# Optimization experiments

Measured on AMD Instinct MI355X. Metric: run time of the kernel, lower is better.

## Reference

```python
import jax, jax.numpy as jnp
import numpy as np

B, S, D, H, E, K = 4, 2048, 768, 3072, 8, 2
CAP_FACTOR = 1.5


def setup_inputs() -> dict:
    key = jax.random.key(0)
    ks = jax.random.split(key, 6)
    x = jax.random.normal(ks[0], (B, S, D), jnp.float32)
    Wr = jax.random.normal(ks[1], (D, E), jnp.float32) * 0.01  # router, std=0.01 init
    w1 = jax.random.normal(ks[2], (E, D, H), jnp.float32) * (1.0 / np.sqrt(D))
    b1 = jnp.zeros((E, H), jnp.float32)
    w2 = jax.random.normal(ks[3], (E, H, D), jnp.float32) * (1.0 / np.sqrt(H))
    b2 = jnp.zeros((E, D), jnp.float32)
    return {"x": x, "Wr": Wr, "w1": w1, "b1": b1, "w2": w2, "b2": b2}


def _moe_forward(x, Wr, w1, b1, w2, b2):
    Bz, Sz, Dz = x.shape
    Ez = Wr.shape[1]
    capacity = int((Bz * Sz / Ez) * CAP_FACTOR)  # 1536

    # --- Router (eval mode: no jitter, no dropout) ---
    logits = x @ Wr                                # [B,S,E]
    probs = jax.nn.softmax(logits, axis=-1)
    topk_p, topk_i = jax.lax.top_k(probs, K)       # [B,S,K]
    topk_p = topk_p / topk_p.sum(-1, keepdims=True)

    # --- Capacity-limited assignment, vectorized equivalent of the serial
    #     (b, s, i) loop: an entry is kept iff fewer than `capacity` earlier
    #     entries (in flat (b,s,i) order) chose the same expert. ---
    e_flat = topk_i.reshape(-1)                    # [N], N = B*S*K, i innermost
    p_flat = topk_p.reshape(-1)
    onehot = (e_flat[:, None] == jnp.arange(Ez)[None, :]).astype(x.dtype)  # [N,E]
    counts_before = jnp.cumsum(onehot, axis=0) - onehot                     # [N,E]
    pos = jnp.take_along_axis(counts_before, e_flat[:, None], axis=1)[:, 0]
    keep = (pos < capacity).astype(x.dtype)        # [N]

    # combine weight per (token, expert): sum over the k slots
    cw = (onehot * (p_flat * keep)[:, None]).reshape(Bz, Sz, K, Ez).sum(2)  # [B,S,E]

    # --- Expert FFNs (dense: every expert on every token, weighted combine) ---
    hidden = jax.nn.gelu(jnp.einsum('bsd,edh->bseh', x, w1) + b1, approximate=False)
    expert_out = jnp.einsum('bseh,ehd->bsed', hidden, w2) + b2               # [B,S,E,D]
    return jnp.einsum('bse,bsed->bsd', cw, expert_out)


def reference(x, Wr, w1, b1, w2, b2):
    return _moe_forward(x, Wr, w1, b1, w2, b2)
```

## Files before the change

### kernel.cpp

```cpp
#include <hip/hip_runtime.h>
#include <hip/hip_bf16.h>
#include <math.h>

#define TOK    8192
#define DMODEL 768
#define HDIM   3072
#define NEXP   8
#define CAP    1536
#define NFLAT  (TOK*2)

typedef __attribute__((ext_vector_type(8))) short bf16x8;
typedef __attribute__((ext_vector_type(4))) float f32x4;

static __device__ __forceinline__ unsigned short f2bf(float f) {
  unsigned int u = __float_as_uint(f);
  u += 0x7FFF + ((u >> 16) & 1);
  return (unsigned short)(u >> 16);
}

static __device__ __forceinline__ float fast_gelu(float v) {
  const float v2 = v * v;
  const float y2 = v * (1.59576912f + 0.07135534f * v2);
  const float e  = __expf(y2);
  return v - v * __builtin_amdgcn_rcpf(e + 1.0f);
}

__global__ __launch_bounds__(256)
void moe_router(const float* __restrict__ x, const float* __restrict__ Wr,
                int* __restrict__ eidx, float* __restrict__ pw)
{
  const int wid = threadIdx.x >> 6, lane = threadIdx.x & 63;
  const int t = blockIdx.x * 4 + wid;
  const float* xr = x + (size_t)t * DMODEL;
  double acc[NEXP];
#pragma unroll
  for (int e = 0; e < NEXP; ++e) acc[e] = 0.0;
  for (int j = 0; j < DMODEL / 64; ++j) {
    const int d = j * 64 + lane;
    const double xv = (double)xr[d];
    const float* wrow = Wr + (size_t)d * NEXP;
#pragma unroll
    for (int e = 0; e < NEXP; ++e) acc[e] += xv * (double)wrow[e];
  }
#pragma unroll
  for (int off = 32; off > 0; off >>= 1) {
#pragma unroll
    for (int e = 0; e < NEXP; ++e) acc[e] += __shfl_xor(acc[e], off, 64);
  }
  if (lane == 0) {
    int e0 = 0;
    for (int e = 1; e < NEXP; ++e) if (acc[e] > acc[e0]) e0 = e;
    int e1 = (e0 == 0) ? 1 : 0;
    for (int e = 0; e < NEXP; ++e) { if (e == e0) continue; if (acc[e] > acc[e1]) e1 = e; }
    const double p0 = 1.0 / (1.0 + exp(acc[e1] - acc[e0]));
    eidx[t * 2 + 0] = e0; eidx[t * 2 + 1] = e1;
    pw[t * 2 + 0] = (float)p0; pw[t * 2 + 1] = (float)(1.0 - p0);
  }
}

__global__ __launch_bounds__(256)
void moe_assign(const int* __restrict__ eidx, int* __restrict__ slotpos,
                int* __restrict__ elist, int* __restrict__ counts)
{
  const int e = blockIdx.x;
  const int tid = threadIdx.x;
  const int base = tid * 64;
  int cnt = 0;
  for (int j = 0; j < 64; ++j) cnt += (eidx[base + j] == e);
  const int lane = tid & 63, wid = tid >> 6;
  int incl = cnt;
  for (int off = 1; off < 64; off <<= 1) {
    int u = __shfl_up(incl, off, 64);
    if (lane >= off) incl += u;
  }
  __shared__ int wsum[4];
  if (lane == 63) wsum[wid] = incl;
  __syncthreads();
  int wbase = 0;
  for (int w = 0; w < wid; ++w) wbase += wsum[w];
  int run = wbase + incl - cnt;
  for (int j = 0; j < 64; ++j) {
    const int n = base + j;
    if (eidx[n] == e) {
      const int pos = run++;
      slotpos[n] = (pos < CAP) ? pos : -1;
      if (pos < CAP) elist[e * CAP + pos] = n >> 1;
    }
  }
  if (tid == 255) {
    int tot = wbase + incl;
    counts[e] = (tot < CAP) ? tot : CAP;
  }
}

__global__ __launch_bounds__(256)
void transpose_bf16(const float* __restrict__ in, unsigned short* __restrict__ out,
                    int R, int C)
{
  __shared__ unsigned short tile[64][65];
  const int e = blockIdx.z;
  in  += (size_t)e * R * C;
  out += (size_t)e * C * R;
  const int c0 = blockIdx.x * 64;
  const int r0 = blockIdx.y * 64;
  const int tid = threadIdx.x;
#pragma unroll
  for (int i = 0; i < 16; ++i) {
    const int L = tid + i * 256;
    const int r = L >> 6, c = L & 63;
    tile[r][c] = f2bf(in[(size_t)(r0 + r) * C + c0 + c]);
  }
  __syncthreads();
#pragma unroll
  for (int i = 0; i < 16; ++i) {
    const int L = tid + i * 256;
    const int rr = L & 63, cc = L >> 6;
    out[(size_t)(c0 + cc) * R + r0 + rr] = tile[rr][cc];
  }
}

__global__ __launch_bounds__(64)
void moe_gather(const float* __restrict__ x, const int* __restrict__ elist,
                const int* __restrict__ counts, unsigned short* __restrict__ Xg)
{
  const int p = blockIdx.x, e = blockIdx.y;
  const int lane = threadIdx.x;
  unsigned short* dst = Xg + ((size_t)e * CAP + p) * DMODEL;
  if (p >= counts[e]) {
    ushort4 z; z.x = z.y = z.z = z.w = 0;
#pragma unroll
    for (int j = 0; j < 3; ++j) ((ushort4*)dst)[j * 64 + lane] = z;
    return;
  }
  const int tok = elist[e * CAP + p];
  const float4* src = (const float4*)(x + (size_t)tok * DMODEL);
#pragma unroll
  for (int j = 0; j < 3; ++j) {
    float4 v = src[j * 64 + lane];
    ushort4 o;
    o.x = f2bf(v.x); o.y = f2bf(v.y); o.z = f2bf(v.z); o.w = f2bf(v.w);
    ((ushort4*)dst)[j * 64 + lane] = o;
  }
}

template <int EPI, int ORD>
__global__ __launch_bounds__(256)
void moe_rs(const unsigned short* __restrict__ Ag, int lda,
            const unsigned short* __restrict__ Bg, int ldb,
            void* __restrict__ Cout0, void* __restrict__ Cout1, int ldc,
            const float* __restrict__ bias,
            int Nsize, int NT, int MT, int NTN)
{
  __shared__ __align__(16) unsigned short lds[2 * 8192];
  unsigned short* const ldsA = lds;
  unsigned short* const ldsB = lds + 8192;

  const int cpx = gridDim.x >> 3;
  const int swz = (blockIdx.x & 7) * cpx + (blockIdx.x >> 3);
  const int e  = swz / cpx;
  int rd = swz - e * cpx;
  int mt, nt, ks;
  if (ORD == 0) { mt = rd % MT;  rd /= MT;  nt = rd % NTN; ks = rd / NTN; }
  else          { nt = rd % NTN; rd /= NTN; mt = rd % MT;  ks = rd / MT;  }
  const int m0 = mt * 128, n0 = nt * 128;
  const int kb = ks * NT * 64;

  const unsigned short* Ae = Ag + (size_t)e * CAP * lda;
  const unsigned short* Be = Bg + (size_t)e * Nsize * ldb;

  const int tid = threadIdx.x, lane = tid & 63, wid = tid >> 6;
  const int wr = wid >> 1, wc = wid & 1;
  const int r16 = lane & 15, g4 = lane >> 4;

  const int srow  = tid >> 3;
  const int scol  = tid & 7;
  const int scolX = scol ^ (srow & 7);
  const unsigned short* pA = Ae + (size_t)(m0 + srow) * lda + scol * 8 + kb;
  const unsigned short* pB = Be + (size_t)(n0 + srow) * ldb + scol * 8 + kb;
  unsigned short* qA = &ldsA[srow * 64 + scolX * 8];
  unsigned short* qB = &ldsB[srow * 64 + scolX * 8];

  float4 a0, a1, a2, a3, b0, b1, b2, b3;

#define LOADT(tt) do {                                                        \
    const size_t ko = (size_t)(tt) * 64;                                      \
    a0 = *(const float4*)(pA + ko);                                           \
    a1 = *(const float4*)(pA + ko + (size_t)32 * lda);                        \
    a2 = *(const float4*)(pA + ko + (size_t)64 * lda);                        \
    a3 = *(const float4*)(pA + ko + (size_t)96 * lda);                        \
    b0 = *(const float4*)(pB + ko);                                           \
    b1 = *(const float4*)(pB + ko + (size_t)32 * ldb);                        \
    b2 = *(const float4*)(pB + ko + (size_t)64 * ldb);                        \
    b3 = *(const float4*)(pB + ko + (size_t)96 * ldb);                        \
  } while (0)

#define STORET() do {                                                         \
    *(float4*)(qA)        = a0;  *(float4*)(qA + 2048) = a1;                  \
    *(float4*)(qA + 4096) = a2;  *(float4*)(qA + 6144) = a3;                  \
    *(float4*)(qB)        = b0;  *(float4*)(qB + 2048) = b1;                  \
    *(float4*)(qB + 4096) = b2;  *(float4*)(qB + 6144) = b3;                  \
  } while (0)

  f32x4 acc[4][4];
#pragma unroll
  for (int i = 0; i < 4; ++i)
#pragma unroll
    for (int j = 0; j < 4; ++j) acc[i][j] = (f32x4){0.f, 0.f, 0.f, 0.f};

  const int cx0 = (g4 ^ (r16 & 7)) * 8;
  const int rA = (wr * 64 + r16) * 64;
  const int rB = (wc * 64 + r16) * 64;

  LOADT(0);
  for (int t = 0; t < NT; ++t) {
    __syncthreads();
    STORET();
    if (t + 1 < NT) LOADT(t + 1);
    __syncthreads();
#pragma unroll
    for (int kh = 0; kh < 2; ++kh) {
      const int cx = cx0 ^ (kh * 32);
      bf16x8 aF[4], bF[4];
#pragma unroll
      for (int mi = 0; mi < 4; ++mi)
        aF[mi] = *(const bf16x8*)&ldsA[rA + mi * 1024 + cx];
#pragma unroll
      for (int ni = 0; ni < 4; ++ni)
        bF[ni] = *(const bf16x8*)&ldsB[rB + ni * 1024 + cx];
#pragma unroll
      for (int mi = 0; mi < 4; ++mi)
#pragma unroll
        for (int ni = 0; ni < 4; ++ni)
          acc[mi][ni] = __builtin_amdgcn_mfma_f32_16x16x32_bf16(aF[mi], bF[ni], acc[mi][ni], 0, 0, 0);
    }
  }
#undef LOADT
#undef STORET

  const float* bvec = bias + (size_t)e * Nsize;
  if constexpr (EPI == 0) {
    __syncthreads();
#pragma unroll
    for (int ni = 0; ni < 4; ++ni) {
      const int lc = wc * 64 + ni * 16 + r16;
      const float bv = bvec[n0 + lc];
#pragma unroll
      for (int mi = 0; mi < 4; ++mi) {
        const int lr0 = wr * 64 + mi * 16 + 4 * g4;
#pragma unroll
        for (int reg = 0; reg < 4; ++reg) {
          lds[(lr0 + reg) * 128 + lc] = f2bf(fast_gelu(acc[mi][ni][reg] + bv));
        }
      }
    }
    __syncthreads();
    unsigned short* C = (unsigned short*)Cout0 + (size_t)e * CAP * ldc;
#pragma unroll
    for (int it = 0; it < 8; ++it) {
      const int chunk = it * 256 + tid;
      const int row = chunk >> 4, c8 = chunk & 15;
      *(float4*)(C + (size_t)(m0 + row) * ldc + n0 + c8 * 8) = *(const float4*)&lds[chunk * 8];
    }
  } else {
    float* C = (float*)(ks ? Cout1 : Cout0) + (size_t)e * CAP * ldc;
#pragma unroll
    for (int ni = 0; ni < 4; ++ni) {
      const int gc = n0 + wc * 64 + ni * 16 + r16;
#pragma unroll
      for (int mi = 0; mi < 4; ++mi) {
        const int gr0 = m0 + wr * 64 + mi * 16 + 4 * g4;
#pragma unroll
        for (int reg = 0; reg < 4; ++reg)
          C[(size_t)(gr0 + reg) * ldc + gc] = acc[mi][ni][reg];
      }
    }
  }
}

__global__ __launch_bounds__(192)
void moe_combine(const float* __restrict__ Y0, const float* __restrict__ Y1,
                 const float* __restrict__ b2, const int* __restrict__ eidx,
                 const float* __restrict__ pw, const int* __restrict__ slotpos,
                 float* __restrict__ out)
{
  const int t = blockIdx.x;
  const int tid = threadIdx.x;
  float4 acc; acc.x = acc.y = acc.z = acc.w = 0.f;
#pragma unroll
  for (int s = 0; s < 2; ++s) {
    const int pos = slotpos[t * 2 + s];
    if (pos >= 0) {
      const int e = eidx[t * 2 + s];
      const float w = pw[t * 2 + s];
      const size_t ro = ((size_t)e * CAP + pos) * DMODEL;
      float4 y0 = ((const float4*)(Y0 + ro))[tid];
      float4 y1 = ((const float4*)(Y1 + ro))[tid];
      float4 bv = ((const float4*)(b2 + (size_t)e * DMODEL))[tid];
      acc.x += w * (y0.x + y1.x + bv.x);
      acc.y += w * (y0.y + y1.y + bv.y);
      acc.z += w * (y0.z + y1.z + bv.z);
      acc.w += w * (y0.w + y1.w + bv.w);
    }
  }
  ((float4*)out)[(size_t)t * (DMODEL / 4) + tid] = acc;
}

extern "C" void kernel_launch(void* const* d_in, const int* in_sizes, int n_in,
                              void* d_out, int out_size, void* d_ws, size_t ws_size,
                              hipStream_t stream)
{
  const float* x  = (const float*)d_in[0];
  const float* Wr = (const float*)d_in[1];
  const float* w1 = (const float*)d_in[2];
  const float* b1 = (const float*)d_in[3];
  const float* w2 = (const float*)d_in[4];
  const float* b2 = (const float*)d_in[5];
  float* out = (float*)d_out;

  char* ws = (char*)d_ws;
  const size_t SZ_W1T = (size_t)NEXP * HDIM * DMODEL * 2;
  const size_t SZ_W2T = (size_t)NEXP * DMODEL * HDIM * 2;
  const size_t SZ_XG  = (size_t)NEXP * CAP * DMODEL * 2;
  const size_t SZ_H   = (size_t)NEXP * CAP * HDIM * 2;
  const size_t SZ_Y   = (size_t)NEXP * CAP * DMODEL * 4;
  unsigned short* w1t = (unsigned short*)(ws);               size_t off = SZ_W1T;
  unsigned short* w2t = (unsigned short*)(ws + off);         off += SZ_W2T;
  unsigned short* Xg  = (unsigned short*)(ws + off);         off += SZ_XG;
  unsigned short* Hb  = (unsigned short*)(ws + off);         off += SZ_H;
  float*          Y0  = (float*)(ws + off);                  off += SZ_Y;
  int*   eidx    = (int*)(ws + off);                         off += (size_t)TOK * 2 * 4;
  float* pw      = (float*)(ws + off);                       off += (size_t)TOK * 2 * 4;
  int*   slotpos = (int*)(ws + off);                         off += (size_t)NFLAT * 4;
  int*   elist   = (int*)(ws + off);                         off += (size_t)NEXP * CAP * 4;
  int*   counts  = (int*)(ws + off);
  float* Y1 = (float*)w1t;

  moe_router<<<TOK / 4, 256, 0, stream>>>(x, Wr, eidx, pw);
  moe_assign<<<NEXP, 256, 0, stream>>>(eidx, slotpos, elist, counts);
  transpose_bf16<<<dim3(HDIM / 64, DMODEL / 64, NEXP), 256, 0, stream>>>(w1, w1t, DMODEL, HDIM);
  transpose_bf16<<<dim3(DMODEL / 64, HDIM / 64, NEXP), 256, 0, stream>>>(w2, w2t, HDIM, DMODEL);
  moe_gather<<<dim3(CAP, NEXP), 64, 0, stream>>>(x, elist, counts, Xg);
  moe_rs<0, 0><<<2304, 256, 0, stream>>>(
      Xg, DMODEL, w1t, DMODEL, Hb, Hb, HDIM, b1, HDIM, 12, 12, 24);
  moe_rs<1, 1><<<1152, 256, 0, stream>>>(
      Hb, HDIM, w2t, HDIM, Y0, Y1, DMODEL, b2, DMODEL, 24, 12, 6);
  moe_combine<<<TOK, 192, 0, stream>>>(Y0, Y1, b2, eidx, pw, slotpos, out);
}
```

Baseline: 244.7 us.

## Enlarge first expert GEMM tile to 256 rows and vectorize transpose/assign loads

The first expert GEMM now uses 256x128 tiles (MI=8 per wave), halving its grid and doubling reuse of each loaded weight tile. The GELU epilogue writes through LDS in two 128-row passes. The weight transpose kernel now uses float4 loads and ushort4 stores, and the assign kernel reads expert indices as int4. The larger tile raises accumulator register pressure (128 floats per thread) and LDS use, which may lower occupancy.

Result: slower. 730.6 us (+198.5%).

```diff
diff --git a/kernel.cpp b/kernel.cpp
--- a/kernel.cpp
+++ b/kernel.cpp
@@ -65,8 +65,13 @@
   const int e = blockIdx.x;
   const int tid = threadIdx.x;
   const int base = tid * 64;
+  const int4* p4 = (const int4*)(eidx + base);
   int cnt = 0;
-  for (int j = 0; j < 64; ++j) cnt += (eidx[base + j] == e);
+#pragma unroll
+  for (int j = 0; j < 16; ++j) {
+    int4 v = p4[j];
+    cnt += (v.x == e) + (v.y == e) + (v.z == e) + (v.w == e);
+  }
   const int lane = tid & 63, wid = tid >> 6;
   int incl = cnt;
   for (int off = 1; off < 64; off <<= 1) {
@@ -79,12 +84,18 @@
   int wbase = 0;
   for (int w = 0; w < wid; ++w) wbase += wsum[w];
   int run = wbase + incl - cnt;
-  for (int j = 0; j < 64; ++j) {
-    const int n = base + j;
-    if (eidx[n] == e) {
-      const int pos = run++;
-      slotpos[n] = (pos < CAP) ? pos : -1;
-      if (pos < CAP) elist[e * CAP + pos] = n >> 1;
+#pragma unroll
+  for (int j = 0; j < 16; ++j) {
+    int4 v = p4[j];
+    const int n = base + j * 4;
+    int vv[4] = {v.x, v.y, v.z, v.w};
+#pragma unroll
+    for (int q = 0; q < 4; ++q) {
+      if (vv[q] == e) {
+        const int pos = run++;
+        slotpos[n + q] = (pos < CAP) ? pos : -1;
+        if (pos < CAP) elist[e * CAP + pos] = (n + q) >> 1;
+      }
     }
   }
   if (tid == 255) {
@@ -101,21 +112,29 @@
   const int e = blockIdx.z;
   in  += (size_t)e * R * C;
   out += (size_t)e * C * R;
-  const int c0 = blockIdx.x * 64;
-  const int r0 = blockIdx.y * 64;
+  const int c0 = blockIdx.x * 64, r0 = blockIdx.y * 64;
   const int tid = threadIdx.x;
-#pragma unroll
-  for (int i = 0; i < 16; ++i) {
-    const int L = tid + i * 256;
-    const int r = L >> 6, c = L & 63;
-    tile[r][c] = f2bf(in[(size_t)(r0 + r) * C + c0 + c]);
+  const int rL = tid >> 4;
+  const int cq = (tid & 15) * 4;
+#pragma unroll
+  for (int p = 0; p < 4; ++p) {
+    const int r = rL + p * 16;
+    float4 v = *(const float4*)&in[(size_t)(r0 + r) * C + c0 + cq];
+    tile[r][cq + 0] = f2bf(v.x);
+    tile[r][cq + 1] = f2bf(v.y);
+    tile[r][cq + 2] = f2bf(v.z);
+    tile[r][cq + 3] = f2bf(v.w);
   }
   __syncthreads();
-#pragma unroll
-  for (int i = 0; i < 16; ++i) {
-    const int L = tid + i * 256;
-    const int rr = L & 63, cc = L >> 6;
-    out[(size_t)(c0 + cc) * R + r0 + rr] = tile[rr][cc];
+  const int cL = tid >> 4;
+  const int rq = (tid & 15) * 4;
+#pragma unroll
+  for (int p = 0; p < 4; ++p) {
+    const int cc = cL + p * 16;
+    ushort4 o;
+    o.x = tile[rq + 0][cc]; o.y = tile[rq + 1][cc];
+    o.z = tile[rq + 2][cc]; o.w = tile[rq + 3][cc];
+    *(ushort4*)&out[(size_t)(c0 + cc) * R + r0 + rq] = o;
   }
 }
 
@@ -143,7 +162,7 @@
   }
 }
 
-template <int EPI, int ORD>
+template <int EPI, int ORD, int MI>
 __global__ __launch_bounds__(256)
 void moe_rs(const unsigned short* __restrict__ Ag, int lda,
             const unsigned short* __restrict__ Bg, int ldb,
@@ -151,9 +170,11 @@
             const float* __restrict__ bias,
             int Nsize, int NT, int MT, int NTN)
 {
-  __shared__ __align__(16) unsigned short lds[2 * 8192];
+  constexpr int BM  = MI * 32;
+  constexpr int ASZ = BM * 64;
+  __shared__ __align__(16) unsigned short lds[ASZ + 8192];
   unsigned short* const ldsA = lds;
-  unsigned short* const ldsB = lds + 8192;
+  unsigned short* const ldsB = lds + ASZ;
 
   const int cpx = gridDim.x >> 3;
   const int swz = (blockIdx.x & 7) * cpx + (blockIdx.x >> 3);
@@ -162,7 +183,7 @@
   int mt, nt, ks;
   if (ORD == 0) { mt = rd % MT;  rd /= MT;  nt = rd % NTN; ks = rd / NTN; }
   else          { nt = rd % NTN; rd /= NTN; mt = rd % MT;  ks = rd / MT;  }
-  const int m0 = mt * 128, n0 = nt * 128;
+  const int m0 = mt * BM, n0 = nt * 128;
   const int kb = ks * NT * 64;
 
   const unsigned short* Ae = Ag + (size_t)e * CAP * lda;
@@ -180,35 +201,29 @@
   unsigned short* qA = &ldsA[srow * 64 + scolX * 8];
   unsigned short* qB = &ldsB[srow * 64 + scolX * 8];
 
-  float4 a0, a1, a2, a3, b0, b1, b2, b3;
-
-#define LOADT(tt) do {                                                        \
-    const size_t ko = (size_t)(tt) * 64;                                      \
-    a0 = *(const float4*)(pA + ko);                                           \
-    a1 = *(const float4*)(pA + ko + (size_t)32 * lda);                        \
-    a2 = *(const float4*)(pA + ko + (size_t)64 * lda);                        \
-    a3 = *(const float4*)(pA + ko + (size_t)96 * lda);                        \
-    b0 = *(const float4*)(pB + ko);                                           \
-    b1 = *(const float4*)(pB + ko + (size_t)32 * ldb);                        \
-    b2 = *(const float4*)(pB + ko + (size_t)64 * ldb);                        \
-    b3 = *(const float4*)(pB + ko + (size_t)96 * ldb);                        \
-  } while (0)
-
-#define STORET() do {                                                         \
-    *(float4*)(qA)        = a0;  *(float4*)(qA + 2048) = a1;                  \
-    *(float4*)(qA + 4096) = a2;  *(float4*)(qA + 6144) = a3;                  \
-    *(float4*)(qB)        = b0;  *(float4*)(qB + 2048) = b1;                  \
-    *(float4*)(qB + 4096) = b2;  *(float4*)(qB + 6144) = b3;                  \
-  } while (0)
-
-  f32x4 acc[4][4];
-#pragma unroll
-  for (int i = 0; i < 4; ++i)
+  float4 a[MI], b[4];
+  auto LOADT = [&](int tt) {
+    const size_t ko = (size_t)tt * 64;
+#pragma unroll
+    for (int j = 0; j < MI; ++j) a[j] = *(const float4*)(pA + ko + (size_t)(32 * j) * lda);
+#pragma unroll
+    for (int j = 0; j < 4; ++j)  b[j] = *(const float4*)(pB + ko + (size_t)(32 * j) * ldb);
+  };
+  auto STORET = [&]() {
+#pragma unroll
+    for (int j = 0; j < MI; ++j) *(float4*)(qA + j * 2048) = a[j];
+#pragma unroll
+    for (int j = 0; j < 4; ++j)  *(float4*)(qB + j * 2048) = b[j];
+  };
+
+  f32x4 acc[MI][4];
+#pragma unroll
+  for (int i = 0; i < MI; ++i)
 #pragma unroll
     for (int j = 0; j < 4; ++j) acc[i][j] = (f32x4){0.f, 0.f, 0.f, 0.f};
 
   const int cx0 = (g4 ^ (r16 & 7)) * 8;
-  const int rA = (wr * 64 + r16) * 64;
+  const int rA = (wr * (MI * 16) + r16) * 64;
   const int rB = (wc * 64 + r16) * 64;
 
   LOADT(0);
@@ -220,46 +235,50 @@
 #pragma unroll
     for (int kh = 0; kh < 2; ++kh) {
       const int cx = cx0 ^ (kh * 32);
-      bf16x8 aF[4], bF[4];
-#pragma unroll
-      for (int mi = 0; mi < 4; ++mi)
+      bf16x8 aF[MI], bF[4];
+#pragma unroll
+      for (int mi = 0; mi < MI; ++mi)
         aF[mi] = *(const bf16x8*)&ldsA[rA + mi * 1024 + cx];
 #pragma unroll
       for (int ni = 0; ni < 4; ++ni)
         bF[ni] = *(const bf16x8*)&ldsB[rB + ni * 1024 + cx];
 #pragma unroll
-      for (int mi = 0; mi < 4; ++mi)
+      for (int mi = 0; mi < MI; ++mi)
 #pragma unroll
         for (int ni = 0; ni < 4; ++ni)
           acc[mi][ni] = __builtin_amdgcn_mfma_f32_16x16x32_bf16(aF[mi], bF[ni], acc[mi][ni], 0, 0, 0);
     }
   }
-#undef LOADT
-#undef STORET
 
   const float* bvec = bias + (size_t)e * Nsize;
   if constexpr (EPI == 0) {
-    __syncthreads();
-#pragma unroll
-    for (int ni = 0; ni < 4; ++ni) {
-      const int lc = wc * 64 + ni * 16 + r16;
-      const float bv = bvec[n0 + lc];
-#pragma unroll
-      for (int mi = 0; mi < 4; ++mi) {
-        const int lr0 = wr * 64 + mi * 16 + 4 * g4;
-#pragma unroll
-        for (int reg = 0; reg < 4; ++reg) {
-          lds[(lr0 + reg) * 128 + lc] = f2bf(fast_gelu(acc[mi][ni][reg] + bv));
+    constexpr int NP = BM / 128;
+#pragma unroll
+    for (int p = 0; p < NP; ++p) {
+      __syncthreads();
+      if (NP == 1 || wr == p) {
+#pragma unroll
+        for (int ni = 0; ni < 4; ++ni) {
+          const int lc = wc * 64 + ni * 16 + r16;
+          const float bv = bvec[n0 + lc];
+#pragma unroll
+          for (int mi = 0; mi < MI; ++mi) {
+            const int lr0 = (NP == 1 ? wr * 64 : 0) + mi * 16 + 4 * g4;
+#pragma unroll
+            for (int reg = 0; reg < 4; ++reg)
+              lds[(lr0 + reg) * 128 + lc] = f2bf(fast_gelu(acc[mi][ni][reg] + bv));
+          }
         }
       }
-    }
-    __syncthreads();
-    unsigned short* C = (unsigned short*)Cout0 + (size_t)e * CAP * ldc;
-#pragma unroll
-    for (int it = 0; it < 8; ++it) {
-      const int chunk = it * 256 + tid;
-      const int row = chunk >> 4, c8 = chunk & 15;
-      *(float4*)(C + (size_t)(m0 + row) * ldc + n0 + c8 * 8) = *(const float4*)&lds[chunk * 8];
+      __syncthreads();
+      unsigned short* C = (unsigned short*)Cout0 + (size_t)e * CAP * ldc;
+#pragma unroll
+      for (int it = 0; it < 8; ++it) {
+        const int chunk = it * 256 + tid;
+        const int row = chunk >> 4, c8 = chunk & 15;
+        *(float4*)(C + (size_t)(m0 + p * 128 + row) * ldc + n0 + c8 * 8) =
+            *(const float4*)&lds[chunk * 8];
+      }
     }
   } else {
     float* C = (float*)(ks ? Cout1 : Cout0) + (size_t)e * CAP * ldc;
@@ -267,8 +286,8 @@
     for (int ni = 0; ni < 4; ++ni) {
       const int gc = n0 + wc * 64 + ni * 16 + r16;
 #pragma unroll
-      for (int mi = 0; mi < 4; ++mi) {
-        const int gr0 = m0 + wr * 64 + mi * 16 + 4 * g4;
+      for (int mi = 0; mi < MI; ++mi) {
+        const int gr0 = m0 + wr * (MI * 16) + mi * 16 + 4 * g4;
 #pragma unroll
         for (int reg = 0; reg < 4; ++reg)
           C[(size_t)(gr0 + reg) * ldc + gc] = acc[mi][ni][reg];
@@ -340,9 +359,9 @@
   transpose_bf16<<<dim3(HDIM / 64, DMODEL / 64, NEXP), 256, 0, stream>>>(w1, w1t, DMODEL, HDIM);
   transpose_bf16<<<dim3(DMODEL / 64, HDIM / 64, NEXP), 256, 0, stream>>>(w2, w2t, HDIM, DMODEL);
   moe_gather<<<dim3(CAP, NEXP), 64, 0, stream>>>(x, elist, counts, Xg);
-  moe_rs<0, 0><<<2304, 256, 0, stream>>>(
-      Xg, DMODEL, w1t, DMODEL, Hb, Hb, HDIM, b1, HDIM, 12, 12, 24);
-  moe_rs<1, 1><<<1152, 256, 0, stream>>>(
+  moe_rs<0, 0, 8><<<1152, 256, 0, stream>>>(
+      Xg, DMODEL, w1t, DMODEL, Hb, Hb, HDIM, b1, HDIM, 12, 6, 24);
+  moe_rs<1, 1, 4><<<1152, 256, 0, stream>>>(
       Hb, HDIM, w2t, HDIM, Y0, Y1, DMODEL, b2, DMODEL, 24, 12, 6);
   moe_combine<<<TOK, 192, 0, stream>>>(Y0, Y1, b2, eidx, pw, slotpos, out);
 }
```
